# Optimization experiments

Measured on AMD Instinct MI355X. Metric: run time of the kernel, lower is better.

The kernel has to match this reference:

```python
import jax, jax.numpy as jnp
import numpy as np

INPUTSIZE = 40
K = 5          # kenrnal_size
STRIDE = 3
KN = 32        # kenrnal_num
LABEL_NODES = 50
BATCH = 64
SAMPLE_NUM = 4


def _build_model():
    """Replicates __init__/create_J_H: dense symmetric Ising coupling J and field H."""
    starts = np.arange(0, INPUTSIZE - K + 1, STRIDE)          # window starts (torch unfold)
    win = starts[:, None] + np.arange(K)                      # [P, K] pixel rows/cols per window
    P = win.shape[0]
    # image_idxs[p] = flattened pixel indices of patch p (row-major over H windows then W windows)
    image_idxs = (win[:, None, :, None] * INPUTSIZE + win[None, :, None, :]).reshape(P * P, K * K)
    cnn_idxs = np.tile(image_idxs, (KN, 1))                   # [cnn_n, K*K]
    cnn_flags = np.repeat(np.arange(KN), P * P)               # kernel id per cnn node

    img_n = INPUTSIZE * INPUTSIZE
    cnn_n = cnn_idxs.shape[0]
    out_n = LABEL_NODES
    N = img_n + cnn_n + out_n

    rng = np.random.default_rng(0)
    J_CNN = (rng.standard_normal((KN, K * K)) * 0.01).astype(np.float32)
    J_MLP = (rng.standard_normal((cnn_n, out_n)) * 0.01).astype(np.float32)
    H = np.concatenate([
        rng.standard_normal(img_n) * 0.01,
        np.zeros(cnn_n),
        rng.standard_normal(out_n) * 0.01,
    ]).astype(np.float32)

    J = np.zeros((N, N), np.float32)
    rows = img_n + np.repeat(np.arange(cnn_n), K * K)
    cols = cnn_idxs.reshape(-1)
    vals = J_CNN[cnn_flags].reshape(-1)
    J[rows, cols] = vals
    J[cols, rows] = vals
    J[img_n:img_n + cnn_n, img_n + cnn_n:] = J_MLP
    J[img_n + cnn_n:, img_n:img_n + cnn_n] = J_MLP.T

    # Graph is bipartite (edges only cnn<->img and cnn<->out): valid 2-coloring.
    group1 = np.arange(img_n, img_n + cnn_n, dtype=np.int64)                      # cnn nodes
    group0 = np.concatenate([np.arange(img_n, dtype=np.int64),
                             np.arange(img_n + cnn_n, N, dtype=np.int64)])        # img + output nodes
    return J, H, group0, group1


def setup_inputs() -> dict:
    J, H, group0, group1 = _build_model()
    key = jax.random.key(0)
    # create_m: random +/-1 spins
    m = jnp.where(jax.random.randint(key, (BATCH, J.shape[0]), 0, 2) == 0, -1.0, 1.0).astype(jnp.float32)
    return {
        "m": m,
        "J": jnp.asarray(J),
        "H": jnp.asarray(H),
        "group0": jnp.asarray(group0),
        "group1": jnp.asarray(group1),
        "sample_num": SAMPLE_NUM,
    }


def reference(m, J, H, group0, group1, sample_num):
    """construct(): sample_num sweeps of per-color-group Gibbs updates.
    Per group: I = J[idxs] @ m.T + H[idxs]; m[:, idxs] = sign(tanh(I) - U(-1,1)).
    """
    keys = jax.random.split(jax.random.key(1), int(sample_num))

    def sweep(m, k):
        k0, k1 = jax.random.split(k)
        for idxs, kk in ((group0, k0), (group1, k1)):
            I = m @ J[idxs].T + H[idxs]                       # [B, |group|]
            u = jax.random.uniform(kk, I.shape, dtype=I.dtype) * 2.0 - 1.0
            m = m.at[:, idxs].set(jnp.sign(jnp.tanh(I) - u))
        return m, None

    m, _ = jax.lax.scan(sweep, m, keys)
    return m


if __name__ == "__main__":
    out = reference(**setup_inputs())
    print(out.shape, out.dtype)
```

## Files before the change

kernel.cpp:

```cpp
#include <hip/hip_runtime.h>
#include <stdint.h>

#define NN     6258
#define IMG_N  1600
#define CNN_N  4608
#define OUT_N  50
#define BATCH  64
#define G0SZ   1650
#define G1SZ   4608
#define IMGW   40
#define NPATCH 12

__host__ __device__ inline void tf2x32(uint32_t k0, uint32_t k1,
                                       uint32_t x0, uint32_t x1,
                                       uint32_t& o0, uint32_t& o1) {
    uint32_t ks[3] = {k0, k1, k0 ^ k1 ^ 0x1BD11BDAu};
    const int rotA[4] = {13, 15, 26, 6};
    const int rotB[4] = {17, 29, 16, 24};
    x0 += ks[0];
    x1 += ks[1];
#pragma unroll
    for (int i = 0; i < 5; ++i) {
        const int* rot = (i & 1) ? rotB : rotA;
#pragma unroll
        for (int j = 0; j < 4; ++j) {
            x0 += x1;
            x1 = (x1 << rot[j]) | (x1 >> (32 - rot[j]));
            x1 ^= x0;
        }
        x0 += ks[(i + 1) % 3];
        x1 += ks[(i + 2) % 3] + (uint32_t)(i + 1);
    }
    o0 = x0;
    o1 = x1;
}

__device__ inline float jax_uniform_pm1(uint32_t k0, uint32_t k1, uint32_t j) {
    uint32_t o0, o1;
    tf2x32(k0, k1, 0u, j, o0, o1);
    uint32_t bits = o0 ^ o1;
    float f = __uint_as_float((bits >> 9) | 0x3f800000u);
    return (f - 1.0f) * 2.0f - 1.0f;
}

__device__ inline float tanh_xla_f32(float x) {
    if (fabsf(x) < 0.0004f) return x;
    float xc = fminf(fmaxf(x, -9.0f), 9.0f);
    float x2 = __fmul_rn(xc, xc);
    float num = -2.76076847742355e-16f;
    num = __fadd_rn(__fmul_rn(num, x2), 2.00018790482477e-13f);
    num = __fadd_rn(__fmul_rn(num, x2), -8.60467152213735e-11f);
    num = __fadd_rn(__fmul_rn(num, x2), 5.12229709037114e-08f);
    num = __fadd_rn(__fmul_rn(num, x2), 1.48572235717979e-05f);
    num = __fadd_rn(__fmul_rn(num, x2), 6.37261928875436e-04f);
    num = __fadd_rn(__fmul_rn(num, x2), 4.89352455891786e-03f);
    num = __fmul_rn(num, xc);
    float den = 1.19825839466702e-06f;
    den = __fadd_rn(__fmul_rn(den, x2), 1.18534705686654e-04f);
    den = __fadd_rn(__fmul_rn(den, x2), 2.26843463243900e-03f);
    den = __fadd_rn(__fmul_rn(den, x2), 4.89352518554385e-03f);
    return __fdiv_rn(num, den);
}

__device__ inline float gibbs_decide(double acc, float h, float u) {
    float I32 = (float)(acc + (double)h);
    float t = tanh_xla_f32(I32);
    float d = __fadd_rn(t, -u);
    return (d > 0.0f) ? 1.0f : ((d < 0.0f) ? -1.0f : 0.0f);
}

__device__ __forceinline__ float jcnn(const float* __restrict__ J, int f, int pos) {
    int a = pos / 5, bb = pos % 5;
    return J[(size_t)(IMG_N + f * 144) * NN + a * IMGW + bb];
}

__global__ __launch_bounds__(256) void t_in(const float* __restrict__ src,
                                            float* __restrict__ dst) {
    int tid = blockIdx.x * 256 + (int)threadIdx.x;
    if (tid < NN * BATCH) {
        int node = tid >> 6, b = tid & 63;
        dst[tid] = src[(size_t)b * NN + node];
    }
}

__global__ __launch_bounds__(256) void t_out(const float* __restrict__ src,
                                             float* __restrict__ dst) {
    int tid = blockIdx.x * 256 + (int)threadIdx.x;
    if (tid < NN * BATCH) {
        int b = tid / NN, node = tid - b * NN;
        dst[tid] = src[node * 64 + b];
    }
}

__global__ __launch_bounds__(256) void g0_kernel(float* __restrict__ mt,
                                                 const float* __restrict__ J,
                                                 const float* __restrict__ H,
                                                 uint32_t k0, uint32_t k1) {
    __shared__ double red[4][64];
    int blk = blockIdx.x;
    if (blk < 400) {
        int tid = blk * 256 + (int)threadIdx.x;
        int g = __builtin_amdgcn_readfirstlane(tid >> 6);
        int b = (int)threadIdx.x & 63;
        int r = g / IMGW, c = g % IMGW;
        int pr_lo = (r >= 4) ? (r - 2) / 3 : 0;
        int pr_hi = r / 3; if (pr_hi > NPATCH - 1) pr_hi = NPATCH - 1;
        int pc_lo = (c >= 4) ? (c - 2) / 3 : 0;
        int pc_hi = c / 3; if (pc_hi > NPATCH - 1) pc_hi = NPATCH - 1;
        double acc = 0.0;
        for (int pr = pr_lo; pr <= pr_hi; ++pr) {
            for (int pc = pc_lo; pc <= pc_hi; ++pc) {
                int pos = (r - 3 * pr) * 5 + (c - 3 * pc);
                int node0 = IMG_N + pr * NPATCH + pc;
#pragma unroll
                for (int f = 0; f < 32; ++f) {
                    float w = jcnn(J, f, pos);
                    acc += (double)w * (double)mt[(node0 + f * 144) * 64 + b];
                }
            }
        }
        float u = jax_uniform_pm1(k0, k1, (uint32_t)(b * G0SZ + g));
        mt[g * 64 + b] = gibbs_decide(acc, H[g], u);
    } else {
        int o = blk - 400;
        int w = (int)threadIdx.x >> 6;
        int lane = (int)threadIdx.x & 63;
        const float* Jrow = J + (size_t)(IMG_N + CNN_N + o) * NN + IMG_N;
        double a0 = 0.0, a1 = 0.0;
        int k0i = w * 1152;
#pragma unroll 4
        for (int k = 0; k < 1152; k += 2) {
            a0 += (double)Jrow[k0i + k]     * (double)mt[(IMG_N + k0i + k) * 64 + lane];
            a1 += (double)Jrow[k0i + k + 1] * (double)mt[(IMG_N + k0i + k + 1) * 64 + lane];
        }
        red[w][lane] = a0 + a1;
        __syncthreads();
        if (w == 0) {
            double a = ((red[0][lane] + red[1][lane]) + red[2][lane]) + red[3][lane];
            float u = jax_uniform_pm1(k0, k1, (uint32_t)(lane * G0SZ + IMG_N + o));
            mt[(IMG_N + CNN_N + o) * 64 + lane] =
                gibbs_decide(a, H[IMG_N + CNN_N + o], u);
        }
    }
}

__global__ __launch_bounds__(256) void g1_kernel(float* __restrict__ mt,
                                                 const float* __restrict__ J,
                                                 const float* __restrict__ H,
                                                 uint32_t k0, uint32_t k1) {
    int tid = blockIdx.x * 256 + (int)threadIdx.x;
    int cnode = __builtin_amdgcn_readfirstlane(tid >> 6);
    int b = (int)threadIdx.x & 63;
    int f = cnode / 144;
    int p = cnode - f * 144;
    int pr = p / NPATCH, pc = p - pr * NPATCH;
    int r0 = pr * 3, c0 = pc * 3;
    double acc = 0.0;
#pragma unroll
    for (int a = 0; a < 5; ++a) {
        int rowbase = (r0 + a) * IMGW + c0;
#pragma unroll
        for (int bb = 0; bb < 5; ++bb) {
            float w = jcnn(J, f, a * 5 + bb);
            acc += (double)w * (double)mt[(rowbase + bb) * 64 + b];
        }
    }
    const float* Jo = J + (size_t)(IMG_N + cnode) * NN + IMG_N + CNN_N;
#pragma unroll 10
    for (int o = 0; o < OUT_N; ++o)
        acc += (double)Jo[o] * (double)mt[(IMG_N + CNN_N + o) * 64 + b];
    float u = jax_uniform_pm1(k0, k1, (uint32_t)(b * G1SZ + cnode));
    mt[(IMG_N + cnode) * 64 + b] = gibbs_decide(acc, H[IMG_N + cnode], u);
}

extern "C" void kernel_launch(void* const* d_in, const int* in_sizes, int n_in,
                              void* d_out, int out_size, void* d_ws, size_t ws_size,
                              hipStream_t stream) {
    const float* m_in = (const float*)d_in[0];
    const float* J    = (const float*)d_in[1];
    const float* H    = (const float*)d_in[2];
    float* m_out = (float*)d_out;
    float* mt    = (float*)d_ws;

    const int TN = (NN * BATCH + 255) / 256;
    t_in<<<TN, 256, 0, stream>>>(m_in, mt);

    uint32_t K[4][2];
    for (int i = 0; i < 4; ++i)
        tf2x32(0u, 1u, 0u, (uint32_t)i, K[i][0], K[i][1]);

    for (int s = 0; s < 4; ++s) {
        uint32_t k0a, k0b, k1a, k1b;
        tf2x32(K[s][0], K[s][1], 0u, 0u, k0a, k0b);
        tf2x32(K[s][0], K[s][1], 0u, 1u, k1a, k1b);
        g0_kernel<<<450, 256, 0, stream>>>(mt, J, H, k0a, k0b);
        g1_kernel<<<1152, 256, 0, stream>>>(mt, J, H, k1a, k1b);
    }

    t_out<<<TN, 256, 0, stream>>>(mt, m_out);
}
```

Before: 380.8 us.

## Fuse all sweeps into one persistent kernel with software grid barriers

Replaces the ten separate launches (transpose-in, two per sweep, transpose-out) with one persistent 256-block kernel that uses an atomic grid barrier between group phases. It also caches the 800 CNN kernel weights in shared memory instead of reading them from scattered rows of J. This removes launch gaps and per-launch overhead. The cost is that fewer waves are resident than in the old grids, and the barrier counters live in the output buffer, which relies on all blocks being co-resident.

```diff
diff --git a/kernel.cpp b/kernel.cpp
--- a/kernel.cpp
+++ b/kernel.cpp
@@ -10,6 +10,7 @@
 #define G1SZ   4608
 #define IMGW   40
 #define NPATCH 12
+#define NB     256
 
 __host__ __device__ inline void tf2x32(uint32_t k0, uint32_t k1,
                                        uint32_t x0, uint32_t x1,
@@ -69,108 +70,131 @@
     return (d > 0.0f) ? 1.0f : ((d < 0.0f) ? -1.0f : 0.0f);
 }
 
-__device__ __forceinline__ float jcnn(const float* __restrict__ J, int f, int pos) {
-    int a = pos / 5, bb = pos % 5;
-    return J[(size_t)(IMG_N + f * 144) * NN + a * IMGW + bb];
-}
-
-__global__ __launch_bounds__(256) void t_in(const float* __restrict__ src,
-                                            float* __restrict__ dst) {
-    int tid = blockIdx.x * 256 + (int)threadIdx.x;
-    if (tid < NN * BATCH) {
-        int node = tid >> 6, b = tid & 63;
-        dst[tid] = src[(size_t)b * NN + node];
-    }
-}
-
-__global__ __launch_bounds__(256) void t_out(const float* __restrict__ src,
-                                             float* __restrict__ dst) {
-    int tid = blockIdx.x * 256 + (int)threadIdx.x;
-    if (tid < NN * BATCH) {
-        int b = tid / NN, node = tid - b * NN;
-        dst[tid] = src[node * 64 + b];
-    }
-}
-
-__global__ __launch_bounds__(256) void g0_kernel(float* __restrict__ mt,
-                                                 const float* __restrict__ J,
-                                                 const float* __restrict__ H,
-                                                 uint32_t k0, uint32_t k1) {
+struct SweepKeys { uint32_t v[16]; };
+
+__global__ __launch_bounds__(64) void zinit(uint32_t* p) {
+    if (threadIdx.x == 0) { p[0] = 0u; p[64] = 0u; }
+}
+
+__device__ __forceinline__ void grid_sync(uint32_t* bar, uint32_t* gen) {
+    __syncthreads();
+    if (threadIdx.x == 0) {
+        uint32_t g = __hip_atomic_load(gen, __ATOMIC_ACQUIRE, __HIP_MEMORY_SCOPE_AGENT);
+        __threadfence();
+        uint32_t arr = __hip_atomic_fetch_add(bar, 1u, __ATOMIC_ACQ_REL,
+                                              __HIP_MEMORY_SCOPE_AGENT);
+        if (arr == (uint32_t)(NB - 1)) {
+            __hip_atomic_store(bar, 0u, __ATOMIC_RELAXED, __HIP_MEMORY_SCOPE_AGENT);
+            __hip_atomic_fetch_add(gen, 1u, __ATOMIC_RELEASE, __HIP_MEMORY_SCOPE_AGENT);
+        } else {
+            while (__hip_atomic_load(gen, __ATOMIC_ACQUIRE,
+                                     __HIP_MEMORY_SCOPE_AGENT) == g)
+                __builtin_amdgcn_s_sleep(1);
+        }
+        __threadfence();
+    }
+    __syncthreads();
+}
+
+__global__ __launch_bounds__(256) void fused(const float* __restrict__ m_in,
+                                             const float* __restrict__ J,
+                                             const float* __restrict__ H,
+                                             float* __restrict__ m_out,
+                                             float* __restrict__ mt,
+                                             SweepKeys keys) {
+    uint32_t* bar = (uint32_t*)m_out;
+    uint32_t* gen = bar + 64;
+    __shared__ float  jc[800];
     __shared__ double red[4][64];
-    int blk = blockIdx.x;
-    if (blk < 400) {
-        int tid = blk * 256 + (int)threadIdx.x;
-        int g = __builtin_amdgcn_readfirstlane(tid >> 6);
-        int b = (int)threadIdx.x & 63;
-        int r = g / IMGW, c = g % IMGW;
-        int pr_lo = (r >= 4) ? (r - 2) / 3 : 0;
-        int pr_hi = r / 3; if (pr_hi > NPATCH - 1) pr_hi = NPATCH - 1;
-        int pc_lo = (c >= 4) ? (c - 2) / 3 : 0;
-        int pc_hi = c / 3; if (pc_hi > NPATCH - 1) pc_hi = NPATCH - 1;
-        double acc = 0.0;
-        for (int pr = pr_lo; pr <= pr_hi; ++pr) {
-            for (int pc = pc_lo; pc <= pc_hi; ++pc) {
-                int pos = (r - 3 * pr) * 5 + (c - 3 * pc);
-                int node0 = IMG_N + pr * NPATCH + pc;
-#pragma unroll
-                for (int f = 0; f < 32; ++f) {
-                    float w = jcnn(J, f, pos);
-                    acc += (double)w * (double)mt[(node0 + f * 144) * 64 + b];
+    const int tid  = (int)threadIdx.x;
+    const int blk  = (int)blockIdx.x;
+    const int lane = tid & 63;
+    const int wave = tid >> 6;
+    const int gwid = blk * 4 + wave;
+
+    for (int t = blk * 256 + tid; t < NN * BATCH; t += NB * 256)
+        mt[t] = m_in[(size_t)(t & 63) * NN + (t >> 6)];
+    for (int t = tid; t < 800; t += 256) {
+        int f = t / 25, pos = t % 25;
+        jc[t] = J[(size_t)(IMG_N + f * 144) * NN + (pos / 5) * IMGW + (pos % 5)];
+    }
+    grid_sync(bar, gen);
+
+    for (int s = 0; s < 4; ++s) {
+        const uint32_t k0a = keys.v[s * 4 + 0], k0b = keys.v[s * 4 + 1];
+        const uint32_t k1a = keys.v[s * 4 + 2], k1b = keys.v[s * 4 + 3];
+
+        if (blk < 50) {
+            const int o = blk;
+            const float* Jrow = J + (size_t)(IMG_N + CNN_N + o) * NN + IMG_N;
+            double a0 = 0.0, a1 = 0.0;
+            const int k0i = wave * 1152;
+#pragma unroll 4
+            for (int k = 0; k < 1152; k += 2) {
+                a0 += (double)Jrow[k0i + k]     * (double)mt[(IMG_N + k0i + k) * 64 + lane];
+                a1 += (double)Jrow[k0i + k + 1] * (double)mt[(IMG_N + k0i + k + 1) * 64 + lane];
+            }
+            red[wave][lane] = a0 + a1;
+            __syncthreads();
+            if (wave == 0) {
+                double a = ((red[0][lane] + red[1][lane]) + red[2][lane]) + red[3][lane];
+                float u = jax_uniform_pm1(k0a, k0b, (uint32_t)(lane * G0SZ + IMG_N + o));
+                mt[(IMG_N + CNN_N + o) * 64 + lane] =
+                    gibbs_decide(a, H[IMG_N + CNN_N + o], u);
+            }
+        } else {
+            const int iw = (blk - 50) * 4 + wave;
+            for (int g = iw; g < IMG_N; g += 824) {
+                int r = g / IMGW, c = g % IMGW;
+                int pr_lo = (r >= 4) ? (r - 2) / 3 : 0;
+                int pr_hi = r / 3; if (pr_hi > NPATCH - 1) pr_hi = NPATCH - 1;
+                int pc_lo = (c >= 4) ? (c - 2) / 3 : 0;
+                int pc_hi = c / 3; if (pc_hi > NPATCH - 1) pc_hi = NPATCH - 1;
+                double acc = 0.0;
+                for (int pr = pr_lo; pr <= pr_hi; ++pr) {
+                    for (int pc = pc_lo; pc <= pc_hi; ++pc) {
+                        int pos = (r - 3 * pr) * 5 + (c - 3 * pc);
+                        int node0 = IMG_N + pr * NPATCH + pc;
+#pragma unroll
+                        for (int f = 0; f < 32; ++f)
+                            acc += (double)jc[f * 25 + pos] *
+                                   (double)mt[(node0 + f * 144) * 64 + lane];
+                    }
                 }
-            }
-        }
-        float u = jax_uniform_pm1(k0, k1, (uint32_t)(b * G0SZ + g));
-        mt[g * 64 + b] = gibbs_decide(acc, H[g], u);
-    } else {
-        int o = blk - 400;
-        int w = (int)threadIdx.x >> 6;
-        int lane = (int)threadIdx.x & 63;
-        const float* Jrow = J + (size_t)(IMG_N + CNN_N + o) * NN + IMG_N;
-        double a0 = 0.0, a1 = 0.0;
-        int k0i = w * 1152;
-#pragma unroll 4
-        for (int k = 0; k < 1152; k += 2) {
-            a0 += (double)Jrow[k0i + k]     * (double)mt[(IMG_N + k0i + k) * 64 + lane];
-            a1 += (double)Jrow[k0i + k + 1] * (double)mt[(IMG_N + k0i + k + 1) * 64 + lane];
-        }
-        red[w][lane] = a0 + a1;
-        __syncthreads();
-        if (w == 0) {
-            double a = ((red[0][lane] + red[1][lane]) + red[2][lane]) + red[3][lane];
-            float u = jax_uniform_pm1(k0, k1, (uint32_t)(lane * G0SZ + IMG_N + o));
-            mt[(IMG_N + CNN_N + o) * 64 + lane] =
-                gibbs_decide(a, H[IMG_N + CNN_N + o], u);
-        }
-    }
-}
-
-__global__ __launch_bounds__(256) void g1_kernel(float* __restrict__ mt,
-                                                 const float* __restrict__ J,
-                                                 const float* __restrict__ H,
-                                                 uint32_t k0, uint32_t k1) {
-    int tid = blockIdx.x * 256 + (int)threadIdx.x;
-    int cnode = __builtin_amdgcn_readfirstlane(tid >> 6);
-    int b = (int)threadIdx.x & 63;
-    int f = cnode / 144;
-    int p = cnode - f * 144;
-    int pr = p / NPATCH, pc = p - pr * NPATCH;
-    int r0 = pr * 3, c0 = pc * 3;
-    double acc = 0.0;
-#pragma unroll
-    for (int a = 0; a < 5; ++a) {
-        int rowbase = (r0 + a) * IMGW + c0;
-#pragma unroll
-        for (int bb = 0; bb < 5; ++bb) {
-            float w = jcnn(J, f, a * 5 + bb);
-            acc += (double)w * (double)mt[(rowbase + bb) * 64 + b];
-        }
-    }
-    const float* Jo = J + (size_t)(IMG_N + cnode) * NN + IMG_N + CNN_N;
+                float u = jax_uniform_pm1(k0a, k0b, (uint32_t)(lane * G0SZ + g));
+                mt[g * 64 + lane] = gibbs_decide(acc, H[g], u);
+            }
+        }
+        grid_sync(bar, gen);
+
+        for (int cn = gwid; cn < CNN_N; cn += NB * 4) {
+            int f = cn / 144;
+            int p = cn - f * 144;
+            int pr = p / NPATCH, pc = p - pr * NPATCH;
+            int r0 = pr * 3, c0 = pc * 3;
+            double acc = 0.0;
+#pragma unroll
+            for (int a = 0; a < 5; ++a) {
+                int rowbase = (r0 + a) * IMGW + c0;
+#pragma unroll
+                for (int bb = 0; bb < 5; ++bb)
+                    acc += (double)jc[f * 25 + a * 5 + bb] *
+                           (double)mt[(rowbase + bb) * 64 + lane];
+            }
+            const float* Jo = J + (size_t)(IMG_N + cn) * NN + IMG_N + CNN_N;
 #pragma unroll 10
-    for (int o = 0; o < OUT_N; ++o)
-        acc += (double)Jo[o] * (double)mt[(IMG_N + CNN_N + o) * 64 + b];
-    float u = jax_uniform_pm1(k0, k1, (uint32_t)(b * G1SZ + cnode));
-    mt[(IMG_N + cnode) * 64 + b] = gibbs_decide(acc, H[IMG_N + cnode], u);
+            for (int o = 0; o < OUT_N; ++o)
+                acc += (double)Jo[o] * (double)mt[(IMG_N + CNN_N + o) * 64 + lane];
+            float u = jax_uniform_pm1(k1a, k1b, (uint32_t)(lane * G1SZ + cn));
+            mt[(IMG_N + cn) * 64 + lane] = gibbs_decide(acc, H[IMG_N + cn], u);
+        }
+        grid_sync(bar, gen);
+    }
+
+    for (int t = blk * 256 + tid; t < NN * BATCH; t += NB * 256) {
+        int b = t / NN, node = t - b * NN;
+        m_out[t] = mt[node * 64 + b];
+    }
 }
 
 extern "C" void kernel_launch(void* const* d_in, const int* in_sizes, int n_in,
@@ -182,20 +206,18 @@
     float* m_out = (float*)d_out;
     float* mt    = (float*)d_ws;
 
-    const int TN = (NN * BATCH + 255) / 256;
-    t_in<<<TN, 256, 0, stream>>>(m_in, mt);
-
     uint32_t K[4][2];
     for (int i = 0; i < 4; ++i)
         tf2x32(0u, 1u, 0u, (uint32_t)i, K[i][0], K[i][1]);
-
+    SweepKeys keys;
     for (int s = 0; s < 4; ++s) {
         uint32_t k0a, k0b, k1a, k1b;
         tf2x32(K[s][0], K[s][1], 0u, 0u, k0a, k0b);
         tf2x32(K[s][0], K[s][1], 0u, 1u, k1a, k1b);
-        g0_kernel<<<450, 256, 0, stream>>>(mt, J, H, k0a, k0b);
-        g1_kernel<<<1152, 256, 0, stream>>>(mt, J, H, k1a, k1b);
-    }
-
-    t_out<<<TN, 256, 0, stream>>>(mt, m_out);
-}
+        keys.v[s * 4 + 0] = k0a; keys.v[s * 4 + 1] = k0b;
+        keys.v[s * 4 + 2] = k1a; keys.v[s * 4 + 3] = k1b;
+    }
+
+    zinit<<<1, 64, 0, stream>>>((uint32_t*)d_out);
+    fused<<<NB, 256, 0, stream>>>(m_in, J, H, m_out, mt, keys);
+}
```

New measurement: 1.262 ms. 3.32x slower.
